# Kernel tuning notes

Hardware: AMD Instinct MI355X
Metric: run time of the kernel (lower is better)

## Reference

```python
import jax, jax.numpy as jnp
import numpy as np

C = 128        # attention channels (inner_channel)
OUT_C = 256    # bottleneck output channels (in_channel)
NEG = -10000000.0


def conv_bn_relu(x, W, scale, shift):
    """1x1 conv (no bias) + eval-mode BatchNorm folded to scale/shift + ReLU.
    x: [B, Cin, H, W], W: [Cout, Cin]."""
    y = jnp.einsum('oc,bchw->bohw', W, x)
    y = y * scale[None, :, None, None] + shift[None, :, None, None]
    return jax.nn.relu(y)


def setup_inputs() -> dict:
    key = jax.random.key(0)
    ks = jax.random.split(key, 20)
    B, H, W_, K = 4, 128, 128, 1024
    inp = {
        'query_feats': jax.random.normal(ks[0], (B, C, H, W_), jnp.float32),
        'key_feats':   jax.random.normal(ks[1], (B, C, K, 1), jnp.float32),
        'value_feats': jax.random.normal(ks[2], (B, C, K, 1), jnp.float32),
        'key_mask':    jax.random.randint(ks[3], (B, 1, K, 1), 0, 2).astype(bool),
    }
    s = 1.0 / np.sqrt(C)

    def mk(i, cin, cout):
        return (jax.random.normal(ks[i], (cout, cin), jnp.float32) * s,
                jnp.ones((cout,), jnp.float32),
                jnp.zeros((cout,), jnp.float32))

    inp['Wq1'], inp['sq1'], inp['bq1'] = mk(4, C, C)
    inp['Wq2'], inp['sq2'], inp['bq2'] = mk(5, C, C)
    inp['Wk1'], inp['sk1'], inp['bk1'] = mk(6, C, C)
    inp['Wk2'], inp['sk2'], inp['bk2'] = mk(7, C, C)
    inp['Wv'],  inp['sv'],  inp['bv']  = mk(8, C, C)
    inp['Wo'],  inp['so'],  inp['bo']  = mk(9, C, C)
    inp['Wb'],  inp['sb'],  inp['bb']  = mk(10, 2 * C, OUT_C)
    return inp


def reference(query_feats, key_feats, value_feats, key_mask,
              Wq1, sq1, bq1, Wq2, sq2, bq2,
              Wk1, sk1, bk1, Wk2, sk2, bk2,
              Wv, sv, bv, Wo, so, bo, Wb, sb, bb):
    B, _, H, W_ = query_feats.shape
    # projections (2 conv-bn-relu for q/k, 1 for v)
    q = conv_bn_relu(conv_bn_relu(query_feats, Wq1, sq1, bq1), Wq2, sq2, bq2)
    k = conv_bn_relu(conv_bn_relu(key_feats, Wk1, sk1, bk1), Wk2, sk2, bk2)
    v = conv_bn_relu(value_feats, Wv, sv, bv)

    q = q.reshape(B, C, -1).transpose(0, 2, 1)   # [B, HW, C]
    k = k.reshape(B, C, -1)                      # [B, C, K]
    v = v.reshape(B, C, -1).transpose(0, 2, 1)   # [B, K, C]

    sim = jnp.einsum('bqc,bck->bqk', q, k) * (C ** -0.5)   # [B, HW, K]
    m = key_mask.reshape(B, 1, -1).astype(sim.dtype)        # [B, 1, K]
    sim = sim * m + NEG * (1.0 - m)
    attn = jax.nn.softmax(sim, axis=-1)

    ctx = jnp.einsum('bqk,bkc->bqc', attn, v)               # [B, HW, C]
    ctx = ctx.transpose(0, 2, 1).reshape(B, C, H, W_)
    ctx = conv_bn_relu(ctx, Wo, so, bo)                     # out_project

    out = conv_bn_relu(jnp.concatenate([ctx, query_feats], axis=1), Wb, sb, bb)
    return out
```

## Files before the change

### kernel.cpp

```cpp
#include <hip/hip_runtime.h>
#include <hip/hip_bf16.h>

#define B_    4
#define C_    128
#define HW_   16384
#define K_    1024
#define NEG_  (-10000000.0f)
#define SCALE_ 0.08838834764831845f

using bf16 = __hip_bfloat16;
typedef __bf16 b8v __attribute__((ext_vector_type(8)));
typedef __bf16 b4v __attribute__((ext_vector_type(4)));
typedef __bf16 b2v __attribute__((ext_vector_type(2)));
typedef float  f4v __attribute__((ext_vector_type(4)));

__device__ __forceinline__ b8v ldb8(const void* p) { return *(const b8v*)p; }
__device__ __forceinline__ b4v ldb4(const void* p) { return *(const b4v*)p; }
__device__ __forceinline__ void storev(float* p, float v) { *p = v; }
__device__ __forceinline__ void storev(bf16* p, float v)  { *p = __float2bfloat16(v); }

#define XSTRIDE 272

__global__ __launch_bounds__(256) void wprep_kernel(
    const float* __restrict__ Wq1, const float* __restrict__ sq1,
    const float* __restrict__ Wq2, const float* __restrict__ sq2,
    const float* __restrict__ Wo,  const float* __restrict__ so,
    const float* __restrict__ Wb,  const float* __restrict__ sb,
    __bf16* __restrict__ Wq1p, __bf16* __restrict__ Wq2p,
    __bf16* __restrict__ Wop,  __bf16* __restrict__ Wbp)
{
    const int idx = blockIdx.x * 256 + threadIdx.x;
    if (idx < 16384)      { Wq1p[idx] = (__bf16)(Wq1[idx] * sq1[idx >> 7]); }
    else if (idx < 32768) { const int i = idx - 16384; Wq2p[i] = (__bf16)(Wq2[i] * sq2[i >> 7]); }
    else if (idx < 49152) { const int i = idx - 32768; Wop[i]  = (__bf16)(Wo[i]  * so[i >> 7]); }
    else                  { const int i = idx - 49152; Wbp[i]  = (__bf16)(Wb[i]  * sb[i >> 8]); }
}

__global__ __launch_bounds__(256) void tq_kernel(const float* __restrict__ query,
                                                 bf16* __restrict__ qt)
{
    __shared__ float Xs[64 * 129];
    const int p0 = blockIdx.x * 64, b = blockIdx.y, t = threadIdx.x;
    const int pl = t & 63, cg = t >> 6;
#pragma unroll 4
    for (int i = 0; i < 32; ++i) {
        const int c = cg * 32 + i;
        Xs[pl * 129 + c] = query[(size_t)(b * 128 + c) * HW_ + p0 + pl];
    }
    __syncthreads();
#pragma unroll 4
    for (int it = 0; it < 16; ++it) {
        const int p = it * 4 + cg;
        b2v pk;
        pk[0] = (__bf16)Xs[p * 129 + 2 * pl];
        pk[1] = (__bf16)Xs[p * 129 + 2 * pl + 1];
        *(b2v*)(qt + ((size_t)b * HW_ + p0 + p) * 128 + 2 * pl) = pk;
    }
}

__device__ __forceinline__ void layer128_lds(const float* __restrict__ Xs, float* __restrict__ Ysh,
                                             const float* __restrict__ W,
                                             const float* __restrict__ sc, const float* __restrict__ sh)
{
    const int t = threadIdx.x;
    const int o = t & 127;
    const int half = t >> 7;
    float acc[16];
#pragma unroll
    for (int p = 0; p < 16; ++p) acc[p] = 0.f;
    const float* wrow  = W + o * 128;
    const float* xbase = Xs + half * 16;
    for (int c = 0; c < 128; c += 4) {
        const float4 w4 = *(const float4*)(wrow + c);
        const float wj[4] = {w4.x, w4.y, w4.z, w4.w};
#pragma unroll
        for (int j = 0; j < 4; ++j) {
            const float* xr = xbase + (c + j) * 33;
#pragma unroll
            for (int p = 0; p < 16; ++p) acc[p] += wj[j] * xr[p];
        }
    }
    const float s = sc[o], h = sh[o];
    float* yb = Ysh + o * 33 + half * 16;
#pragma unroll
    for (int p = 0; p < 16; ++p) yb[p] = fmaxf(fmaf(s, acc[p], h), 0.f);
}

template <typename OutT>
__device__ __forceinline__ void layer128_store(const float* __restrict__ Xs, OutT* __restrict__ outp,
                                               const float* __restrict__ W,
                                               const float* __restrict__ sc, const float* __restrict__ sh)
{
    const int t = threadIdx.x;
    const int o = t & 127;
    const int half = t >> 7;
    float acc[16];
#pragma unroll
    for (int p = 0; p < 16; ++p) acc[p] = 0.f;
    const float* wrow  = W + o * 128;
    const float* xbase = Xs + half * 16;
    for (int c = 0; c < 128; c += 4) {
        const float4 w4 = *(const float4*)(wrow + c);
        const float wj[4] = {w4.x, w4.y, w4.z, w4.w};
#pragma unroll
        for (int j = 0; j < 4; ++j) {
            const float* xr = xbase + (c + j) * 33;
#pragma unroll
            for (int p = 0; p < 16; ++p) acc[p] += wj[j] * xr[p];
        }
    }
    const float s = sc[o], h = sh[o];
#pragma unroll
    for (int p = 0; p < 16; ++p) {
        float v = fmaxf(fmaf(s, acc[p], h), 0.f);
        storev(&outp[(size_t)(half * 16 + p) * 128 + o], v);
    }
}

__global__ __launch_bounds__(256) void kv_proj_kernel(
    const float* __restrict__ key, const float* __restrict__ val,
    const float* __restrict__ Wk1, const float* __restrict__ sk1, const float* __restrict__ bk1,
    const float* __restrict__ Wk2, const float* __restrict__ sk2, const float* __restrict__ bk2,
    const float* __restrict__ Wv,  const float* __restrict__ sv,  const float* __restrict__ bv,
    bf16* __restrict__ kbuf, bf16* __restrict__ vbuf)
{
    __shared__ __align__(16) float X[128 * 33];
    __shared__ __align__(16) float Y[128 * 33];
    const int p0 = blockIdx.x * 32;
    const int b  = blockIdx.y;
    const int t  = threadIdx.x;

    for (int e = t; e < 4096; e += 256) {
        int c = e >> 5, p = e & 31;
        X[c * 33 + p] = key[(size_t)(b * 128 + c) * K_ + p0 + p];
    }
    __syncthreads();
    layer128_lds(X, Y, Wk1, sk1, bk1);
    __syncthreads();
    layer128_store(Y, kbuf + (size_t)(b * K_ + p0) * 128, Wk2, sk2, bk2);
    __syncthreads();
    for (int e = t; e < 4096; e += 256) {
        int c = e >> 5, p = e & 31;
        X[c * 33 + p] = val[(size_t)(b * 128 + c) * K_ + p0 + p];
    }
    __syncthreads();
    layer128_lds(X, Y, Wv, sv, bv);
    __syncthreads();
    for (int e = t; e < 4096; e += 256) {
        int c = e >> 5, p = e & 31;
        vbuf[(size_t)(b * 128 + c) * K_ + p0 + p] = __float2bfloat16(Y[c * 33 + p]);
    }
}

__global__ __launch_bounds__(256, 2) void qproj_kernel(
    const bf16* __restrict__ qt,
    const __bf16* __restrict__ W1, const float* __restrict__ sh1,
    const __bf16* __restrict__ W2, const float* __restrict__ sh2,
    bf16* __restrict__ qbuf)
{
    __shared__ __align__(16) char Xs[128 * XSTRIDE];
    __shared__ __align__(16) __bf16 Ys[128 * 136];
    const int t = threadIdx.x, w = t >> 6, lane = t & 63;
    const int pl = lane & 15, quad = lane >> 4;
    const int n0 = blockIdx.x * 128, b = blockIdx.y;
    const int ob = 32 * w;

    {
        const char* qg = (const char*)(qt + ((size_t)b * HW_ + n0) * 128) + t * 16;
        char* xl = Xs + (t >> 4) * XSTRIDE + (t & 15) * 16;
#pragma unroll
        for (int i = 0; i < 8; ++i)
            *(float4*)(xl + i * 16 * XSTRIDE) = *(const float4*)(qg + i * 4096);
    }

    b8v W1f[2][4], W2f[2][4];
#pragma unroll
    for (int mt = 0; mt < 2; ++mt)
#pragma unroll
        for (int s = 0; s < 4; ++s) {
            W1f[mt][s] = ldb8(W1 + (ob + mt * 16 + pl) * 128 + s * 32 + quad * 8);
            W2f[mt][s] = ldb8(W2 + (ob + mt * 16 + pl) * 128 + s * 32 + quad * 8);
        }
    __syncthreads();

    f4v acc[2][8];
#pragma unroll
    for (int mt = 0; mt < 2; ++mt)
#pragma unroll
        for (int nt = 0; nt < 8; ++nt) acc[mt][nt] = (f4v){0.f, 0.f, 0.f, 0.f};

#pragma unroll
    for (int s = 0; s < 4; ++s) {
        b8v Bf[8];
#pragma unroll
        for (int nt = 0; nt < 8; ++nt)
            Bf[nt] = ldb8(Xs + (nt * 16 + pl) * XSTRIDE + s * 64 + quad * 16);
#pragma unroll
        for (int mt = 0; mt < 2; ++mt)
#pragma unroll
            for (int nt = 0; nt < 8; ++nt)
                acc[mt][nt] = __builtin_amdgcn_mfma_f32_16x16x32_bf16(W1f[mt][s], Bf[nt], acc[mt][nt], 0, 0, 0);
    }

#pragma unroll
    for (int mt = 0; mt < 2; ++mt) {
        const float4 s4 = *(const float4*)(sh1 + ob + mt * 16 + quad * 4);
        const float shf[4] = {s4.x, s4.y, s4.z, s4.w};
#pragma unroll
        for (int nt = 0; nt < 8; ++nt) {
            b4v y;
#pragma unroll
            for (int r = 0; r < 4; ++r) y[r] = (__bf16)fmaxf(acc[mt][nt][r] + shf[r], 0.f);
            *(b4v*)&Ys[(nt * 16 + pl) * 136 + ob + mt * 16 + quad * 4] = y;
        }
    }
    __syncthreads();

    f4v acc2[2][8];
#pragma unroll
    for (int mt = 0; mt < 2; ++mt)
#pragma unroll
        for (int nt = 0; nt < 8; ++nt) acc2[mt][nt] = (f4v){0.f, 0.f, 0.f, 0.f};

#pragma unroll
    for (int s = 0; s < 4; ++s) {
        b8v Bf[8];
#pragma unroll
        for (int nt = 0; nt < 8; ++nt)
            Bf[nt] = *(const b8v*)&Ys[(nt * 16 + pl) * 136 + s * 32 + quad * 8];
#pragma unroll
        for (int mt = 0; mt < 2; ++mt)
#pragma unroll
            for (int nt = 0; nt < 8; ++nt)
                acc2[mt][nt] = __builtin_amdgcn_mfma_f32_16x16x32_bf16(W2f[mt][s], Bf[nt], acc2[mt][nt], 0, 0, 0);
    }

    bf16* qb = qbuf + ((size_t)b * HW_ + n0) * 128;
#pragma unroll
    for (int mt = 0; mt < 2; ++mt) {
        const float4 s4 = *(const float4*)(sh2 + ob + mt * 16 + quad * 4);
        const float shf[4] = {s4.x, s4.y, s4.z, s4.w};
#pragma unroll
        for (int nt = 0; nt < 8; ++nt) {
            b4v y;
#pragma unroll
            for (int r = 0; r < 4; ++r) y[r] = (__bf16)fmaxf(acc2[mt][nt][r] + shf[r], 0.f);
            *(b4v*)(qb + (size_t)(nt * 16 + pl) * 128 + ob + mt * 16 + quad * 4) = y;
        }
    }
}

#define KSTRIDE 272
#define VSTRIDE 136
__global__ __launch_bounds__(256, 2) void attn_kernel(
    const bf16* __restrict__ qbuf, const bf16* __restrict__ kbuf, const bf16* __restrict__ vbuf,
    const int* __restrict__ mask, bf16* __restrict__ ctxbuf)
{
    __shared__ __align__(16) float bias[K_];
    __shared__ __align__(16) char ktile[64 * KSTRIDE];
    __shared__ __align__(16) char vtile[128 * VSTRIDE];

    const int t    = threadIdx.x;
    const int w    = t >> 6;
    const int lane = t & 63;
    const int m    = lane & 15;
    const int quad = lane >> 4;
    const int q0   = blockIdx.x * 64;
    const int b    = blockIdx.y;

    for (int i = t; i < K_; i += 256)
        bias[i] = (mask[b * K_ + i] != 0) ? 0.f : NEG_;

    b8v qf[4];
    {
        const bf16* qrow = qbuf + ((size_t)b * HW_ + q0 + w * 16 + m) * 128;
#pragma unroll
        for (int s = 0; s < 4; ++s) qf[s] = ldb8(qrow + s * 32 + quad * 8);
    }

    const bf16* kpt = kbuf + (size_t)b * K_ * 128;
    const bf16* vpt = vbuf + (size_t)b * 128 * K_;

    const char* kg = (const char*)kpt + t * 16;
    const char* vg = (const char*)(vpt + (size_t)(t >> 3) * K_) + (t & 7) * 16;
    char* kl = ktile + (t >> 4) * KSTRIDE + (t & 15) * 16;
    char* vl = vtile + (t >> 3) * VSTRIDE + (t & 7) * 16;

    float4 k_r0 = *(const float4*)(kg);
    float4 k_r1 = *(const float4*)(kg + 4096);
    float4 k_r2 = *(const float4*)(kg + 8192);
    float4 k_r3 = *(const float4*)(kg + 12288);
    float4 v_r0 = *(const float4*)(vg);
    float4 v_r1 = *(const float4*)(vg + 65536);
    float4 v_r2 = *(const float4*)(vg + 131072);
    float4 v_r3 = *(const float4*)(vg + 196608);

    f4v acc[8];
#pragma unroll
    for (int i = 0; i < 8; ++i) acc[i] = (f4v){0.f, 0.f, 0.f, 0.f};
    float mrun = -3.0e38f, lrun = 0.f;

    for (int chunk = 0; chunk < 16; ++chunk) {
        const int k0 = chunk * 64;

        *(float4*)(kl)                = k_r0;
        *(float4*)(kl + 16 * KSTRIDE) = k_r1;
        *(float4*)(kl + 32 * KSTRIDE) = k_r2;
        *(float4*)(kl + 48 * KSTRIDE) = k_r3;
        *(float4*)(vl)                = v_r0;
        *(float4*)(vl + 32 * VSTRIDE) = v_r1;
        *(float4*)(vl + 64 * VSTRIDE) = v_r2;
        *(float4*)(vl + 96 * VSTRIDE) = v_r3;
        __syncthreads();

        if (chunk < 15) {
            const char* kgn = kg + (chunk + 1) * 16384;
            const char* vgn = vg + (chunk + 1) * 128;
            k_r0 = *(const float4*)(kgn);
            k_r1 = *(const float4*)(kgn + 4096);
            k_r2 = *(const float4*)(kgn + 8192);
            k_r3 = *(const float4*)(kgn + 12288);
            v_r0 = *(const float4*)(vgn);
            v_r1 = *(const float4*)(vgn + 65536);
            v_r2 = *(const float4*)(vgn + 131072);
            v_r3 = *(const float4*)(vgn + 196608);
        }

        f4v sv[4];
#pragma unroll
        for (int kt = 0; kt < 4; ++kt) {
            f4v a = (f4v){0.f, 0.f, 0.f, 0.f};
            const char* krow = ktile + (kt * 16 + m) * KSTRIDE + quad * 16;
#pragma unroll
            for (int s = 0; s < 4; ++s)
                a = __builtin_amdgcn_mfma_f32_16x16x32_bf16(ldb8(krow + s * 64), qf[s], a, 0, 0, 0);
            const float4 b4 = *(const float4*)&bias[k0 + kt * 16 + quad * 4];
            const float bb4[4] = {b4.x, b4.y, b4.z, b4.w};
#pragma unroll
            for (int r = 0; r < 4; ++r) sv[kt][r] = a[r] * SCALE_ + bb4[r];
        }

        float mloc = sv[0][0];
#pragma unroll
        for (int kt = 0; kt < 4; ++kt)
#pragma unroll
            for (int r = 0; r < 4; ++r) mloc = fmaxf(mloc, sv[kt][r]);
        mloc = fmaxf(mloc, __shfl_xor(mloc, 16, 64));
        mloc = fmaxf(mloc, __shfl_xor(mloc, 32, 64));
        const float mn = fmaxf(mrun, mloc);
        const float alpha = __expf(mrun - mn);
        mrun = mn;

        b4v pk[4];
        float rs = 0.f;
#pragma unroll
        for (int kt = 0; kt < 4; ++kt)
#pragma unroll
            for (int r = 0; r < 4; ++r) {
                const float p = __expf(sv[kt][r] - mn);
                rs += p;
                pk[kt][r] = (__bf16)p;
            }
        rs += __shfl_xor(rs, 16, 64);
        rs += __shfl_xor(rs, 32, 64);
        lrun = lrun * alpha + rs;

        float alr[4];
#pragma unroll
        for (int r = 0; r < 4; ++r) alr[r] = __shfl(alpha, quad * 4 + r, 64);
#pragma unroll
        for (int ct = 0; ct < 8; ++ct)
#pragma unroll
            for (int r = 0; r < 4; ++r) acc[ct][r] *= alr[r];

        const b8v A0 = __builtin_shufflevector(pk[0], pk[1], 0, 1, 2, 3, 4, 5, 6, 7);
        const b8v A1 = __builtin_shufflevector(pk[2], pk[3], 0, 1, 2, 3, 4, 5, 6, 7);
#pragma unroll
        for (int ct = 0; ct < 8; ++ct) {
            const char* vrow = vtile + (ct * 16 + m) * VSTRIDE + quad * 8;
            const b8v B0 = __builtin_shufflevector(ldb4(vrow),      ldb4(vrow + 32), 0, 1, 2, 3, 4, 5, 6, 7);
            const b8v B1 = __builtin_shufflevector(ldb4(vrow + 64), ldb4(vrow + 96), 0, 1, 2, 3, 4, 5, 6, 7);
            acc[ct] = __builtin_amdgcn_mfma_f32_16x16x32_bf16(A0, B0, acc[ct], 0, 0, 0);
            acc[ct] = __builtin_amdgcn_mfma_f32_16x16x32_bf16(A1, B1, acc[ct], 0, 0, 0);
        }
        __syncthreads();
    }

    float inv[4];
#pragma unroll
    for (int r = 0; r < 4; ++r) inv[r] = 1.f / __shfl(lrun, quad * 4 + r, 64);
    bf16* crow = ctxbuf + ((size_t)b * HW_ + q0 + w * 16) * 128;
#pragma unroll
    for (int ct = 0; ct < 8; ++ct)
#pragma unroll
        for (int r = 0; r < 4; ++r)
            crow[(size_t)(quad * 4 + r) * 128 + ct * 16 + m] = __float2bfloat16(acc[ct][r] * inv[r]);
}

__global__ __launch_bounds__(256, 2) void final_kernel(
    const bf16* __restrict__ ctx, const bf16* __restrict__ qt,
    const __bf16* __restrict__ Wop, const float* __restrict__ bo,
    const __bf16* __restrict__ Wbp, const float* __restrict__ bb,
    float* __restrict__ out)
{
    __shared__ __align__(16) char Xs[128 * XSTRIDE];
    __shared__ __align__(16) __bf16 Ys[128 * 136];
    const int t = threadIdx.x, w = t >> 6, lane = t & 63;
    const int pl = lane & 15, quad = lane >> 4;
    const int n0 = blockIdx.x * 128, b = blockIdx.y;
    const int ob = 32 * w;

    char* xl = Xs + (t >> 4) * XSTRIDE + (t & 15) * 16;

    {
        const char* cg = (const char*)(ctx + ((size_t)b * HW_ + n0) * 128) + t * 16;
#pragma unroll
        for (int i = 0; i < 8; ++i)
            *(float4*)(xl + i * 16 * XSTRIDE) = *(const float4*)(cg + i * 4096);
    }

    b8v Wof[2][4];
#pragma unroll
    for (int mt = 0; mt < 2; ++mt)
#pragma unroll
        for (int s = 0; s < 4; ++s)
            Wof[mt][s] = ldb8(Wop + (ob + mt * 16 + pl) * 128 + s * 32 + quad * 8);
    __syncthreads();

    const char* qg = (const char*)(qt + ((size_t)b * HW_ + n0) * 128) + t * 16;
    float4 q_s0 = *(const float4*)(qg);
    float4 q_s1 = *(const float4*)(qg + 4096);
    float4 q_s2 = *(const float4*)(qg + 8192);
    float4 q_s3 = *(const float4*)(qg + 12288);
    float4 q_s4 = *(const float4*)(qg + 16384);
    float4 q_s5 = *(const float4*)(qg + 20480);
    float4 q_s6 = *(const float4*)(qg + 24576);
    float4 q_s7 = *(const float4*)(qg + 28672);

    f4v acc1[2][8];
#pragma unroll
    for (int mt = 0; mt < 2; ++mt)
#pragma unroll
        for (int nt = 0; nt < 8; ++nt) acc1[mt][nt] = (f4v){0.f, 0.f, 0.f, 0.f};

#pragma unroll
    for (int s = 0; s < 4; ++s) {
        b8v Bf[8];
#pragma unroll
        for (int nt = 0; nt < 8; ++nt)
            Bf[nt] = ldb8(Xs + (nt * 16 + pl) * XSTRIDE + s * 64 + quad * 16);
#pragma unroll
        for (int mt = 0; mt < 2; ++mt)
#pragma unroll
            for (int nt = 0; nt < 8; ++nt)
                acc1[mt][nt] = __builtin_amdgcn_mfma_f32_16x16x32_bf16(Wof[mt][s], Bf[nt], acc1[mt][nt], 0, 0, 0);
    }

#pragma unroll
    for (int mt = 0; mt < 2; ++mt) {
        const float4 s4 = *(const float4*)(bo + ob + mt * 16 + quad * 4);
        const float shf[4] = {s4.x, s4.y, s4.z, s4.w};
#pragma unroll
        for (int nt = 0; nt < 8; ++nt) {
            b4v y;
#pragma unroll
            for (int r = 0; r < 4; ++r) y[r] = (__bf16)fmaxf(acc1[mt][nt][r] + shf[r], 0.f);
            *(b4v*)&Ys[(nt * 16 + pl) * 136 + ob + mt * 16 + quad * 4] = y;
        }
    }
    __syncthreads();

    *(float4*)(xl)                 = q_s0;
    *(float4*)(xl + 16 * XSTRIDE)  = q_s1;
    *(float4*)(xl + 32 * XSTRIDE)  = q_s2;
    *(float4*)(xl + 48 * XSTRIDE)  = q_s3;
    *(float4*)(xl + 64 * XSTRIDE)  = q_s4;
    *(float4*)(xl + 80 * XSTRIDE)  = q_s5;
    *(float4*)(xl + 96 * XSTRIDE)  = q_s6;
    *(float4*)(xl + 112 * XSTRIDE) = q_s7;
    __syncthreads();

    f4v acc2[4][8];
#pragma unroll
    for (int mt = 0; mt < 4; ++mt)
#pragma unroll
        for (int nt = 0; nt < 8; ++nt) acc2[mt][nt] = (f4v){0.f, 0.f, 0.f, 0.f};

#pragma unroll
    for (int ks = 0; ks < 8; ++ks) {
        b8v Af[4];
#pragma unroll
        for (int mt = 0; mt < 4; ++mt)
            Af[mt] = ldb8(Wbp + (64 * w + mt * 16 + pl) * 256 + ks * 32 + quad * 8);
        b8v Bf[8];
        if (ks < 4) {
#pragma unroll
            for (int nt = 0; nt < 8; ++nt)
                Bf[nt] = *(const b8v*)&Ys[(nt * 16 + pl) * 136 + ks * 32 + quad * 8];
        } else {
#pragma unroll
            for (int nt = 0; nt < 8; ++nt)
                Bf[nt] = ldb8(Xs + (nt * 16 + pl) * XSTRIDE + (ks - 4) * 64 + quad * 16);
        }
#pragma unroll
        for (int mt = 0; mt < 4; ++mt)
#pragma unroll
            for (int nt = 0; nt < 8; ++nt)
                acc2[mt][nt] = __builtin_amdgcn_mfma_f32_16x16x32_bf16(Af[mt], Bf[nt], acc2[mt][nt], 0, 0, 0);
    }

#pragma unroll
    for (int mt = 0; mt < 4; ++mt) {
        const float4 s4 = *(const float4*)(bb + 64 * w + mt * 16 + quad * 4);
        const float shf[4] = {s4.x, s4.y, s4.z, s4.w};
#pragma unroll
        for (int nt = 0; nt < 8; ++nt)
#pragma unroll
            for (int r = 0; r < 4; ++r)
                out[(size_t)(b * 256 + 64 * w + mt * 16 + quad * 4 + r) * HW_ + n0 + nt * 16 + pl]
                    = fmaxf(acc2[mt][nt][r] + shf[r], 0.f);
    }
}

extern "C" void kernel_launch(void* const* d_in, const int* in_sizes, int n_in,
                              void* d_out, int out_size, void* d_ws, size_t ws_size,
                              hipStream_t stream)
{
    const float* query = (const float*)d_in[0];
    const float* key   = (const float*)d_in[1];
    const float* val   = (const float*)d_in[2];
    const int*   mask  = (const int*)  d_in[3];
    const float* Wq1 = (const float*)d_in[4];  const float* sq1 = (const float*)d_in[5];  const float* bq1 = (const float*)d_in[6];
    const float* Wq2 = (const float*)d_in[7];  const float* sq2 = (const float*)d_in[8];  const float* bq2 = (const float*)d_in[9];
    const float* Wk1 = (const float*)d_in[10]; const float* sk1 = (const float*)d_in[11]; const float* bk1 = (const float*)d_in[12];
    const float* Wk2 = (const float*)d_in[13]; const float* sk2 = (const float*)d_in[14]; const float* bk2 = (const float*)d_in[15];
    const float* Wv  = (const float*)d_in[16]; const float* sv  = (const float*)d_in[17]; const float* bv  = (const float*)d_in[18];
    const float* Wo  = (const float*)d_in[19]; const float* so  = (const float*)d_in[20]; const float* bo  = (const float*)d_in[21];
    const float* Wb  = (const float*)d_in[22]; const float* sb  = (const float*)d_in[23]; const float* bb  = (const float*)d_in[24];

    char* ws = (char*)d_ws;
    bf16*   kbuf = (bf16*)(ws);
    bf16*   vbuf = (bf16*)(ws + (1u << 20));
    bf16*   qbuf = (bf16*)(ws + (2u << 20));
    bf16*   ctxb = (bf16*)(ws + (18u << 20));
    bf16*   qt   = (bf16*)(ws + (34u << 20));
    __bf16* Wq1p = (__bf16*)(ws + (50u << 20));
    __bf16* Wq2p = (__bf16*)(ws + (50u << 20) + (32u << 10));
    __bf16* Wop  = (__bf16*)(ws + (50u << 20) + (64u << 10));
    __bf16* Wbp  = (__bf16*)(ws + (50u << 20) + (96u << 10));
    float* outp = (float*)d_out;

    wprep_kernel<<<448, 256, 0, stream>>>(Wq1, sq1, Wq2, sq2, Wo, so, Wb, sb,
                                          Wq1p, Wq2p, Wop, Wbp);
    tq_kernel<<<dim3(HW_ / 64, B_), 256, 0, stream>>>(query, qt);
    kv_proj_kernel<<<dim3(K_ / 32, B_), 256, 0, stream>>>(
        key, val, Wk1, sk1, bk1, Wk2, sk2, bk2, Wv, sv, bv, kbuf, vbuf);
    qproj_kernel<<<dim3(HW_ / 128, B_), 256, 0, stream>>>(
        qt, Wq1p, bq1, Wq2p, bq2, qbuf);
    attn_kernel<<<dim3(HW_ / 64, B_), 256, 0, stream>>>(
        qbuf, kbuf, vbuf, mask, ctxb);
    final_kernel<<<dim3(HW_ / 128, B_), 256, 0, stream>>>(
        ctxb, qt, Wop, bo, Wbp, bb, outp);
}
```

Baseline: 269.2 us.

## Merge prep kernels into one launch and split final GEMM into two halves

Folds the weight-prep, query-transpose and key/value projection kernels into a single block-indexed prep kernel, removing two launches and letting the independent work run concurrently. In the final kernel, the 256-row bottleneck GEMM is split into two sequential 128-row halves, with each wave holding its Wb fragments for all k-steps in registers. This lowers accumulator register pressure, which may help occupancy, but the Ys/Xs B-fragments are now read twice from LDS. The merged prep kernel uses 33KB of shared memory for every block, including the transpose and weight blocks, which may lower their occupancy.

```diff
diff --git a/kernel.cpp b/kernel.cpp
--- a/kernel.cpp
+++ b/kernel.cpp
@@ -21,43 +21,6 @@
 
 #define XSTRIDE 272
 
-__global__ __launch_bounds__(256) void wprep_kernel(
-    const float* __restrict__ Wq1, const float* __restrict__ sq1,
-    const float* __restrict__ Wq2, const float* __restrict__ sq2,
-    const float* __restrict__ Wo,  const float* __restrict__ so,
-    const float* __restrict__ Wb,  const float* __restrict__ sb,
-    __bf16* __restrict__ Wq1p, __bf16* __restrict__ Wq2p,
-    __bf16* __restrict__ Wop,  __bf16* __restrict__ Wbp)
-{
-    const int idx = blockIdx.x * 256 + threadIdx.x;
-    if (idx < 16384)      { Wq1p[idx] = (__bf16)(Wq1[idx] * sq1[idx >> 7]); }
-    else if (idx < 32768) { const int i = idx - 16384; Wq2p[i] = (__bf16)(Wq2[i] * sq2[i >> 7]); }
-    else if (idx < 49152) { const int i = idx - 32768; Wop[i]  = (__bf16)(Wo[i]  * so[i >> 7]); }
-    else                  { const int i = idx - 49152; Wbp[i]  = (__bf16)(Wb[i]  * sb[i >> 8]); }
-}
-
-__global__ __launch_bounds__(256) void tq_kernel(const float* __restrict__ query,
-                                                 bf16* __restrict__ qt)
-{
-    __shared__ float Xs[64 * 129];
-    const int p0 = blockIdx.x * 64, b = blockIdx.y, t = threadIdx.x;
-    const int pl = t & 63, cg = t >> 6;
-#pragma unroll 4
-    for (int i = 0; i < 32; ++i) {
-        const int c = cg * 32 + i;
-        Xs[pl * 129 + c] = query[(size_t)(b * 128 + c) * HW_ + p0 + pl];
-    }
-    __syncthreads();
-#pragma unroll 4
-    for (int it = 0; it < 16; ++it) {
-        const int p = it * 4 + cg;
-        b2v pk;
-        pk[0] = (__bf16)Xs[p * 129 + 2 * pl];
-        pk[1] = (__bf16)Xs[p * 129 + 2 * pl + 1];
-        *(b2v*)(qt + ((size_t)b * HW_ + p0 + p) * 128 + 2 * pl) = pk;
-    }
-}
-
 __device__ __forceinline__ void layer128_lds(const float* __restrict__ Xs, float* __restrict__ Ysh,
                                              const float* __restrict__ W,
                                              const float* __restrict__ sc, const float* __restrict__ sh)
@@ -117,38 +80,73 @@
     }
 }
 
-__global__ __launch_bounds__(256) void kv_proj_kernel(
-    const float* __restrict__ key, const float* __restrict__ val,
+__global__ __launch_bounds__(256) void prep_kernel(
+    const float* __restrict__ query, const float* __restrict__ key, const float* __restrict__ val,
     const float* __restrict__ Wk1, const float* __restrict__ sk1, const float* __restrict__ bk1,
     const float* __restrict__ Wk2, const float* __restrict__ sk2, const float* __restrict__ bk2,
     const float* __restrict__ Wv,  const float* __restrict__ sv,  const float* __restrict__ bv,
-    bf16* __restrict__ kbuf, bf16* __restrict__ vbuf)
-{
-    __shared__ __align__(16) float X[128 * 33];
-    __shared__ __align__(16) float Y[128 * 33];
-    const int p0 = blockIdx.x * 32;
-    const int b  = blockIdx.y;
-    const int t  = threadIdx.x;
-
-    for (int e = t; e < 4096; e += 256) {
-        int c = e >> 5, p = e & 31;
-        X[c * 33 + p] = key[(size_t)(b * 128 + c) * K_ + p0 + p];
-    }
-    __syncthreads();
-    layer128_lds(X, Y, Wk1, sk1, bk1);
-    __syncthreads();
-    layer128_store(Y, kbuf + (size_t)(b * K_ + p0) * 128, Wk2, sk2, bk2);
-    __syncthreads();
-    for (int e = t; e < 4096; e += 256) {
-        int c = e >> 5, p = e & 31;
-        X[c * 33 + p] = val[(size_t)(b * 128 + c) * K_ + p0 + p];
-    }
-    __syncthreads();
-    layer128_lds(X, Y, Wv, sv, bv);
-    __syncthreads();
-    for (int e = t; e < 4096; e += 256) {
-        int c = e >> 5, p = e & 31;
-        vbuf[(size_t)(b * 128 + c) * K_ + p0 + p] = __float2bfloat16(Y[c * 33 + p]);
+    const float* __restrict__ Wq1, const float* __restrict__ sq1,
+    const float* __restrict__ Wq2, const float* __restrict__ sq2,
+    const float* __restrict__ Wo,  const float* __restrict__ so,
+    const float* __restrict__ Wb,  const float* __restrict__ sb,
+    bf16* __restrict__ qt, bf16* __restrict__ kbuf, bf16* __restrict__ vbuf,
+    __bf16* __restrict__ Wq1p, __bf16* __restrict__ Wq2p,
+    __bf16* __restrict__ Wop,  __bf16* __restrict__ Wbp)
+{
+    __shared__ __align__(16) float S[2 * 128 * 33];
+    const int blk = blockIdx.x;
+    const int t   = threadIdx.x;
+
+    if (blk < 1024) {
+        float* Xs = S;
+        const int p0 = (blk & 255) * 64, b = blk >> 8;
+        const int pl = t & 63, cg = t >> 6;
+#pragma unroll 4
+        for (int i = 0; i < 32; ++i) {
+            const int c = cg * 32 + i;
+            Xs[pl * 129 + c] = query[(size_t)(b * 128 + c) * HW_ + p0 + pl];
+        }
+        __syncthreads();
+#pragma unroll 4
+        for (int it = 0; it < 16; ++it) {
+            const int p = it * 4 + cg;
+            b2v pk;
+            pk[0] = (__bf16)Xs[p * 129 + 2 * pl];
+            pk[1] = (__bf16)Xs[p * 129 + 2 * pl + 1];
+            *(b2v*)(qt + ((size_t)b * HW_ + p0 + p) * 128 + 2 * pl) = pk;
+        }
+    } else if (blk < 1152) {
+        float* X = S;
+        float* Y = S + 128 * 33;
+        const int local = blk - 1024;
+        const int p0 = (local & 31) * 32, b = local >> 5;
+
+        for (int e = t; e < 4096; e += 256) {
+            int c = e >> 5, p = e & 31;
+            X[c * 33 + p] = key[(size_t)(b * 128 + c) * K_ + p0 + p];
+        }
+        __syncthreads();
+        layer128_lds(X, Y, Wk1, sk1, bk1);
+        __syncthreads();
+        layer128_store(Y, kbuf + (size_t)(b * K_ + p0) * 128, Wk2, sk2, bk2);
+        __syncthreads();
+        for (int e = t; e < 4096; e += 256) {
+            int c = e >> 5, p = e & 31;
+            X[c * 33 + p] = val[(size_t)(b * 128 + c) * K_ + p0 + p];
+        }
+        __syncthreads();
+        layer128_lds(X, Y, Wv, sv, bv);
+        __syncthreads();
+        for (int e = t; e < 4096; e += 256) {
+            int c = e >> 5, p = e & 31;
+            vbuf[(size_t)(b * 128 + c) * K_ + p0 + p] = __float2bfloat16(Y[c * 33 + p]);
+        }
+    } else {
+        const int idx = (blk - 1152) * 256 + t;
+        if (idx < 16384)      { Wq1p[idx] = (__bf16)(Wq1[idx] * sq1[idx >> 7]); }
+        else if (idx < 32768) { const int i = idx - 16384; Wq2p[i] = (__bf16)(Wq2[i] * sq2[i >> 7]); }
+        else if (idx < 49152) { const int i = idx - 32768; Wop[i]  = (__bf16)(Wo[i]  * so[i >> 7]); }
+        else                  { const int i = idx - 49152; Wbp[i]  = (__bf16)(Wb[i]  * sb[i >> 8]); }
     }
 }
 
@@ -480,45 +478,53 @@
     *(float4*)(xl + 112 * XSTRIDE) = q_s7;
     __syncthreads();
 
-    f4v acc2[4][8];
-#pragma unroll
-    for (int mt = 0; mt < 4; ++mt)
-#pragma unroll
-        for (int nt = 0; nt < 8; ++nt) acc2[mt][nt] = (f4v){0.f, 0.f, 0.f, 0.f};
-
-#pragma unroll
-    for (int ks = 0; ks < 8; ++ks) {
-        b8v Af[4];
-#pragma unroll
-        for (int mt = 0; mt < 4; ++mt)
-            Af[mt] = ldb8(Wbp + (64 * w + mt * 16 + pl) * 256 + ks * 32 + quad * 8);
-        b8v Bf[8];
-        if (ks < 4) {
+#pragma unroll 1
+    for (int h = 0; h < 2; ++h) {
+        const int mb = 128 * h + 32 * w;
+
+        b8v Wf[2][8];
+#pragma unroll
+        for (int mt = 0; mt < 2; ++mt)
+#pragma unroll
+            for (int ks = 0; ks < 8; ++ks)
+                Wf[mt][ks] = ldb8(Wbp + (size_t)(mb + mt * 16 + pl) * 256 + ks * 32 + quad * 8);
+
+        f4v acc2[2][8];
+#pragma unroll
+        for (int mt = 0; mt < 2; ++mt)
+#pragma unroll
+            for (int nt = 0; nt < 8; ++nt) acc2[mt][nt] = (f4v){0.f, 0.f, 0.f, 0.f};
+
+#pragma unroll
+        for (int ks = 0; ks < 8; ++ks) {
+            b8v Bf[8];
+            if (ks < 4) {
+#pragma unroll
+                for (int nt = 0; nt < 8; ++nt)
+                    Bf[nt] = *(const b8v*)&Ys[(nt * 16 + pl) * 136 + ks * 32 + quad * 8];
+            } else {
+#pragma unroll
+                for (int nt = 0; nt < 8; ++nt)
+                    Bf[nt] = ldb8(Xs + (nt * 16 + pl) * XSTRIDE + (ks - 4) * 64 + quad * 16);
+            }
+#pragma unroll
+            for (int mt = 0; mt < 2; ++mt)
+#pragma unroll
+                for (int nt = 0; nt < 8; ++nt)
+                    acc2[mt][nt] = __builtin_amdgcn_mfma_f32_16x16x32_bf16(Wf[mt][ks], Bf[nt], acc2[mt][nt], 0, 0, 0);
+        }
+
+#pragma unroll
+        for (int mt = 0; mt < 2; ++mt) {
+            const float4 s4 = *(const float4*)(bb + mb + mt * 16 + quad * 4);
+            const float shf[4] = {s4.x, s4.y, s4.z, s4.w};
 #pragma unroll
             for (int nt = 0; nt < 8; ++nt)
-                Bf[nt] = *(const b8v*)&Ys[(nt * 16 + pl) * 136 + ks * 32 + quad * 8];
-        } else {
-#pragma unroll
-            for (int nt = 0; nt < 8; ++nt)
-                Bf[nt] = ldb8(Xs + (nt * 16 + pl) * XSTRIDE + (ks - 4) * 64 + quad * 16);
-        }
-#pragma unroll
-        for (int mt = 0; mt < 4; ++mt)
-#pragma unroll
-            for (int nt = 0; nt < 8; ++nt)
-                acc2[mt][nt] = __builtin_amdgcn_mfma_f32_16x16x32_bf16(Af[mt], Bf[nt], acc2[mt][nt], 0, 0, 0);
-    }
-
-#pragma unroll
-    for (int mt = 0; mt < 4; ++mt) {
-        const float4 s4 = *(const float4*)(bb + 64 * w + mt * 16 + quad * 4);
-        const float shf[4] = {s4.x, s4.y, s4.z, s4.w};
-#pragma unroll
-        for (int nt = 0; nt < 8; ++nt)
-#pragma unroll
-            for (int r = 0; r < 4; ++r)
-                out[(size_t)(b * 256 + 64 * w + mt * 16 + quad * 4 + r) * HW_ + n0 + nt * 16 + pl]
-                    = fmaxf(acc2[mt][nt][r] + shf[r], 0.f);
+#pragma unroll
+                for (int r = 0; r < 4; ++r)
+                    out[(size_t)(b * 256 + mb + mt * 16 + quad * 4 + r) * HW_ + n0 + nt * 16 + pl]
+                        = fmaxf(acc2[mt][nt][r] + shf[r], 0.f);
+        }
     }
 }
 
@@ -550,11 +556,11 @@
     __bf16* Wbp  = (__bf16*)(ws + (50u << 20) + (96u << 10));
     float* outp = (float*)d_out;
 
-    wprep_kernel<<<448, 256, 0, stream>>>(Wq1, sq1, Wq2, sq2, Wo, so, Wb, sb,
-                                          Wq1p, Wq2p, Wop, Wbp);
-    tq_kernel<<<dim3(HW_ / 64, B_), 256, 0, stream>>>(query, qt);
-    kv_proj_kernel<<<dim3(K_ / 32, B_), 256, 0, stream>>>(
-        key, val, Wk1, sk1, bk1, Wk2, sk2, bk2, Wv, sv, bv, kbuf, vbuf);
+    prep_kernel<<<1600, 256, 0, stream>>>(
+        query, key, val,
+        Wk1, sk1, bk1, Wk2, sk2, bk2, Wv, sv, bv,
+        Wq1, sq1, Wq2, sq2, Wo, so, Wb, sb,
+        qt, kbuf, vbuf, Wq1p, Wq2p, Wop, Wbp);
     qproj_kernel<<<dim3(HW_ / 128, B_), 256, 0, stream>>>(
         qt, Wq1p, bq1, Wq2p, bq2, qbuf);
     attn_kernel<<<dim3(HW_ / 64, B_), 256, 0, stream>>>(
```

New measurement: 324.3 us. +20.5%, slower.

## Move K/V projections to bf16 MFMA and merge them into the Q projection launch

Applied to the files above, without the earlier changes.

Replaces the scalar fp32 K/V projection kernel with bf16 MFMA matrix-core work that shares a body with the Q projection. Key and value are transposed to bf16 alongside the query in one transpose kernel, and their weights are prepped with scale folding in the same weight-prep kernel. One launch now handles Q blocks and K/V blocks together, which removes a kernel launch and the slow scalar FMA loop. In exchange, K and V are projected from bf16-rounded inputs, costing some precision, and the KV blocks (two chained projections plus a third) run longer than Q blocks, giving uneven tail work.

```diff
diff --git a/kernel.cpp b/kernel.cpp
--- a/kernel.cpp
+++ b/kernel.cpp
@@ -16,8 +16,6 @@
 
 __device__ __forceinline__ b8v ldb8(const void* p) { return *(const b8v*)p; }
 __device__ __forceinline__ b4v ldb4(const void* p) { return *(const b4v*)p; }
-__device__ __forceinline__ void storev(float* p, float v) { *p = v; }
-__device__ __forceinline__ void storev(bf16* p, float v)  { *p = __float2bfloat16(v); }
 
 #define XSTRIDE 272
 
@@ -26,26 +24,39 @@
     const float* __restrict__ Wq2, const float* __restrict__ sq2,
     const float* __restrict__ Wo,  const float* __restrict__ so,
     const float* __restrict__ Wb,  const float* __restrict__ sb,
+    const float* __restrict__ Wk1, const float* __restrict__ sk1,
+    const float* __restrict__ Wk2, const float* __restrict__ sk2,
+    const float* __restrict__ Wv,  const float* __restrict__ sv,
     __bf16* __restrict__ Wq1p, __bf16* __restrict__ Wq2p,
-    __bf16* __restrict__ Wop,  __bf16* __restrict__ Wbp)
+    __bf16* __restrict__ Wop,  __bf16* __restrict__ Wbp,
+    __bf16* __restrict__ Wk1p, __bf16* __restrict__ Wk2p, __bf16* __restrict__ Wvp)
 {
     const int idx = blockIdx.x * 256 + threadIdx.x;
-    if (idx < 16384)      { Wq1p[idx] = (__bf16)(Wq1[idx] * sq1[idx >> 7]); }
-    else if (idx < 32768) { const int i = idx - 16384; Wq2p[i] = (__bf16)(Wq2[i] * sq2[i >> 7]); }
-    else if (idx < 49152) { const int i = idx - 32768; Wop[i]  = (__bf16)(Wo[i]  * so[i >> 7]); }
-    else                  { const int i = idx - 49152; Wbp[i]  = (__bf16)(Wb[i]  * sb[i >> 8]); }
-}
-
-__global__ __launch_bounds__(256) void tq_kernel(const float* __restrict__ query,
-                                                 bf16* __restrict__ qt)
+    if (idx < 16384)       { Wq1p[idx] = (__bf16)(Wq1[idx] * sq1[idx >> 7]); }
+    else if (idx < 32768)  { const int i = idx - 16384;  Wq2p[i] = (__bf16)(Wq2[i] * sq2[i >> 7]); }
+    else if (idx < 49152)  { const int i = idx - 32768;  Wop[i]  = (__bf16)(Wo[i]  * so[i >> 7]); }
+    else if (idx < 114688) { const int i = idx - 49152;  Wbp[i]  = (__bf16)(Wb[i]  * sb[i >> 8]); }
+    else if (idx < 131072) { const int i = idx - 114688; Wk1p[i] = (__bf16)(Wk1[i] * sk1[i >> 7]); }
+    else if (idx < 147456) { const int i = idx - 131072; Wk2p[i] = (__bf16)(Wk2[i] * sk2[i >> 7]); }
+    else                   { const int i = idx - 147456; Wvp[i]  = (__bf16)(Wv[i]  * sv[i >> 7]); }
+}
+
+__global__ __launch_bounds__(256) void txp_kernel(
+    const float* __restrict__ query, const float* __restrict__ key, const float* __restrict__ val,
+    bf16* __restrict__ qt, bf16* __restrict__ kT, bf16* __restrict__ vT)
 {
     __shared__ float Xs[64 * 129];
-    const int p0 = blockIdx.x * 64, b = blockIdx.y, t = threadIdx.x;
+    const int seg = blockIdx.x, b = blockIdx.y, t = threadIdx.x;
+    const float* src; bf16* dst; int L, p0;
+    if (seg < 256)      { src = query; dst = qt; L = HW_; p0 = seg * 64; }
+    else if (seg < 272) { src = key;   dst = kT; L = K_;  p0 = (seg - 256) * 64; }
+    else                { src = val;   dst = vT; L = K_;  p0 = (seg - 272) * 64; }
+
     const int pl = t & 63, cg = t >> 6;
 #pragma unroll 4
     for (int i = 0; i < 32; ++i) {
         const int c = cg * 32 + i;
-        Xs[pl * 129 + c] = query[(size_t)(b * 128 + c) * HW_ + p0 + pl];
+        Xs[pl * 129 + c] = src[(size_t)(b * 128 + c) * L + p0 + pl];
     }
     __syncthreads();
 #pragma unroll 4
@@ -54,133 +65,145 @@
         b2v pk;
         pk[0] = (__bf16)Xs[p * 129 + 2 * pl];
         pk[1] = (__bf16)Xs[p * 129 + 2 * pl + 1];
-        *(b2v*)(qt + ((size_t)b * HW_ + p0 + p) * 128 + 2 * pl) = pk;
-    }
-}
-
-__device__ __forceinline__ void layer128_lds(const float* __restrict__ Xs, float* __restrict__ Ysh,
-                                             const float* __restrict__ W,
-                                             const float* __restrict__ sc, const float* __restrict__ sh)
-{
-    const int t = threadIdx.x;
-    const int o = t & 127;
-    const int half = t >> 7;
-    float acc[16];
-#pragma unroll
-    for (int p = 0; p < 16; ++p) acc[p] = 0.f;
-    const float* wrow  = W + o * 128;
-    const float* xbase = Xs + half * 16;
-    for (int c = 0; c < 128; c += 4) {
-        const float4 w4 = *(const float4*)(wrow + c);
-        const float wj[4] = {w4.x, w4.y, w4.z, w4.w};
-#pragma unroll
-        for (int j = 0; j < 4; ++j) {
-            const float* xr = xbase + (c + j) * 33;
-#pragma unroll
-            for (int p = 0; p < 16; ++p) acc[p] += wj[j] * xr[p];
-        }
-    }
-    const float s = sc[o], h = sh[o];
-    float* yb = Ysh + o * 33 + half * 16;
-#pragma unroll
-    for (int p = 0; p < 16; ++p) yb[p] = fmaxf(fmaf(s, acc[p], h), 0.f);
-}
-
-template <typename OutT>
-__device__ __forceinline__ void layer128_store(const float* __restrict__ Xs, OutT* __restrict__ outp,
-                                               const float* __restrict__ W,
-                                               const float* __restrict__ sc, const float* __restrict__ sh)
-{
-    const int t = threadIdx.x;
-    const int o = t & 127;
-    const int half = t >> 7;
-    float acc[16];
-#pragma unroll
-    for (int p = 0; p < 16; ++p) acc[p] = 0.f;
-    const float* wrow  = W + o * 128;
-    const float* xbase = Xs + half * 16;
-    for (int c = 0; c < 128; c += 4) {
-        const float4 w4 = *(const float4*)(wrow + c);
-        const float wj[4] = {w4.x, w4.y, w4.z, w4.w};
-#pragma unroll
-        for (int j = 0; j < 4; ++j) {
-            const float* xr = xbase + (c + j) * 33;
-#pragma unroll
-            for (int p = 0; p < 16; ++p) acc[p] += wj[j] * xr[p];
-        }
-    }
-    const float s = sc[o], h = sh[o];
-#pragma unroll
-    for (int p = 0; p < 16; ++p) {
-        float v = fmaxf(fmaf(s, acc[p], h), 0.f);
-        storev(&outp[(size_t)(half * 16 + p) * 128 + o], v);
-    }
-}
-
-__global__ __launch_bounds__(256) void kv_proj_kernel(
-    const float* __restrict__ key, const float* __restrict__ val,
-    const float* __restrict__ Wk1, const float* __restrict__ sk1, const float* __restrict__ bk1,
-    const float* __restrict__ Wk2, const float* __restrict__ sk2, const float* __restrict__ bk2,
-    const float* __restrict__ Wv,  const float* __restrict__ sv,  const float* __restrict__ bv,
-    bf16* __restrict__ kbuf, bf16* __restrict__ vbuf)
-{
-    __shared__ __align__(16) float X[128 * 33];
-    __shared__ __align__(16) float Y[128 * 33];
-    const int p0 = blockIdx.x * 32;
-    const int b  = blockIdx.y;
-    const int t  = threadIdx.x;
-
-    for (int e = t; e < 4096; e += 256) {
-        int c = e >> 5, p = e & 31;
-        X[c * 33 + p] = key[(size_t)(b * 128 + c) * K_ + p0 + p];
-    }
-    __syncthreads();
-    layer128_lds(X, Y, Wk1, sk1, bk1);
-    __syncthreads();
-    layer128_store(Y, kbuf + (size_t)(b * K_ + p0) * 128, Wk2, sk2, bk2);
-    __syncthreads();
-    for (int e = t; e < 4096; e += 256) {
-        int c = e >> 5, p = e & 31;
-        X[c * 33 + p] = val[(size_t)(b * 128 + c) * K_ + p0 + p];
-    }
-    __syncthreads();
-    layer128_lds(X, Y, Wv, sv, bv);
-    __syncthreads();
-    for (int e = t; e < 4096; e += 256) {
-        int c = e >> 5, p = e & 31;
-        vbuf[(size_t)(b * 128 + c) * K_ + p0 + p] = __float2bfloat16(Y[c * 33 + p]);
-    }
-}
-
-__global__ __launch_bounds__(256, 2) void qproj_kernel(
-    const bf16* __restrict__ qt,
+        *(b2v*)(dst + ((size_t)b * L + p0 + p) * 128 + 2 * pl) = pk;
+    }
+}
+
+__device__ __forceinline__ void proj2_body(
+    const bf16* __restrict__ src,
     const __bf16* __restrict__ W1, const float* __restrict__ sh1,
     const __bf16* __restrict__ W2, const float* __restrict__ sh2,
-    bf16* __restrict__ qbuf)
+    bf16* __restrict__ dst, char* Xs, __bf16* Ys)
+{
+    const int t = threadIdx.x, w = t >> 6, lane = t & 63;
+    const int pl = lane & 15, quad = lane >> 4;
+    const int ob = 32 * w;
+
+    {
+        const char* sg = (const char*)src + t * 16;
+        char* xl = Xs + (t >> 4) * XSTRIDE + (t & 15) * 16;
+#pragma unroll
+        for (int i = 0; i < 8; ++i)
+            *(float4*)(xl + i * 16 * XSTRIDE) = *(const float4*)(sg + i * 4096);
+    }
+
+    b8v W1f[2][4], W2f[2][4];
+#pragma unroll
+    for (int mt = 0; mt < 2; ++mt)
+#pragma unroll
+        for (int s = 0; s < 4; ++s) {
+            W1f[mt][s] = ldb8(W1 + (ob + mt * 16 + pl) * 128 + s * 32 + quad * 8);
+            W2f[mt][s] = ldb8(W2 + (ob + mt * 16 + pl) * 128 + s * 32 + quad * 8);
+        }
+    __syncthreads();
+
+    f4v acc[2][8];
+#pragma unroll
+    for (int mt = 0; mt < 2; ++mt)
+#pragma unroll
+        for (int nt = 0; nt < 8; ++nt) acc[mt][nt] = (f4v){0.f, 0.f, 0.f, 0.f};
+
+#pragma unroll
+    for (int s = 0; s < 4; ++s) {
+        b8v Bf[8];
+#pragma unroll
+        for (int nt = 0; nt < 8; ++nt)
+            Bf[nt] = ldb8(Xs + (nt * 16 + pl) * XSTRIDE + s * 64 + quad * 16);
+#pragma unroll
+        for (int mt = 0; mt < 2; ++mt)
+#pragma unroll
+            for (int nt = 0; nt < 8; ++nt)
+                acc[mt][nt] = __builtin_amdgcn_mfma_f32_16x16x32_bf16(W1f[mt][s], Bf[nt], acc[mt][nt], 0, 0, 0);
+    }
+
+#pragma unroll
+    for (int mt = 0; mt < 2; ++mt) {
+        const float4 s4 = *(const float4*)(sh1 + ob + mt * 16 + quad * 4);
+        const float shf[4] = {s4.x, s4.y, s4.z, s4.w};
+#pragma unroll
+        for (int nt = 0; nt < 8; ++nt) {
+            b4v y;
+#pragma unroll
+            for (int r = 0; r < 4; ++r) y[r] = (__bf16)fmaxf(acc[mt][nt][r] + shf[r], 0.f);
+            *(b4v*)&Ys[(nt * 16 + pl) * 136 + ob + mt * 16 + quad * 4] = y;
+        }
+    }
+    __syncthreads();
+
+    f4v acc2[2][8];
+#pragma unroll
+    for (int mt = 0; mt < 2; ++mt)
+#pragma unroll
+        for (int nt = 0; nt < 8; ++nt) acc2[mt][nt] = (f4v){0.f, 0.f, 0.f, 0.f};
+
+#pragma unroll
+    for (int s = 0; s < 4; ++s) {
+        b8v Bf[8];
+#pragma unroll
+        for (int nt = 0; nt < 8; ++nt)
+            Bf[nt] = *(const b8v*)&Ys[(nt * 16 + pl) * 136 + s * 32 + quad * 8];
+#pragma unroll
+        for (int mt = 0; mt < 2; ++mt)
+#pragma unroll
+            for (int nt = 0; nt < 8; ++nt)
+                acc2[mt][nt] = __builtin_amdgcn_mfma_f32_16x16x32_bf16(W2f[mt][s], Bf[nt], acc2[mt][nt], 0, 0, 0);
+    }
+
+#pragma unroll
+    for (int mt = 0; mt < 2; ++mt) {
+        const float4 s4 = *(const float4*)(sh2 + ob + mt * 16 + quad * 4);
+        const float shf[4] = {s4.x, s4.y, s4.z, s4.w};
+#pragma unroll
+        for (int nt = 0; nt < 8; ++nt) {
+            b4v y;
+#pragma unroll
+            for (int r = 0; r < 4; ++r) y[r] = (__bf16)fmaxf(acc2[mt][nt][r] + shf[r], 0.f);
+            *(b4v*)(dst + (size_t)(nt * 16 + pl) * 128 + ob + mt * 16 + quad * 4) = y;
+        }
+    }
+}
+
+__global__ __launch_bounds__(256, 2) void proj_kernel(
+    const bf16* __restrict__ qt, const bf16* __restrict__ kT, const bf16* __restrict__ vT,
+    const __bf16* __restrict__ Wq1p, const float* __restrict__ bq1,
+    const __bf16* __restrict__ Wq2p, const float* __restrict__ bq2,
+    const __bf16* __restrict__ Wk1p, const float* __restrict__ bk1,
+    const __bf16* __restrict__ Wk2p, const float* __restrict__ bk2,
+    const __bf16* __restrict__ Wvp,  const float* __restrict__ bv,
+    bf16* __restrict__ qbuf, bf16* __restrict__ kbuf, bf16* __restrict__ vbuf)
 {
     __shared__ __align__(16) char Xs[128 * XSTRIDE];
     __shared__ __align__(16) __bf16 Ys[128 * 136];
     const int t = threadIdx.x, w = t >> 6, lane = t & 63;
     const int pl = lane & 15, quad = lane >> 4;
-    const int n0 = blockIdx.x * 128, b = blockIdx.y;
+    const int b = blockIdx.y;
+
+    if (blockIdx.x < 128) {
+        const int n0 = blockIdx.x * 128;
+        proj2_body(qt + ((size_t)b * HW_ + n0) * 128, Wq1p, bq1, Wq2p, bq2,
+                   qbuf + ((size_t)b * HW_ + n0) * 128, Xs, Ys);
+        return;
+    }
+
+    const int n0 = (blockIdx.x - 128) * 128;
+    proj2_body(kT + ((size_t)b * K_ + n0) * 128, Wk1p, bk1, Wk2p, bk2,
+               kbuf + ((size_t)b * K_ + n0) * 128, Xs, Ys);
+    __syncthreads();
+
+    {
+        const char* sg = (const char*)(vT + ((size_t)b * K_ + n0) * 128) + t * 16;
+        char* xl = Xs + (t >> 4) * XSTRIDE + (t & 15) * 16;
+#pragma unroll
+        for (int i = 0; i < 8; ++i)
+            *(float4*)(xl + i * 16 * XSTRIDE) = *(const float4*)(sg + i * 4096);
+    }
     const int ob = 32 * w;
-
-    {
-        const char* qg = (const char*)(qt + ((size_t)b * HW_ + n0) * 128) + t * 16;
-        char* xl = Xs + (t >> 4) * XSTRIDE + (t & 15) * 16;
-#pragma unroll
-        for (int i = 0; i < 8; ++i)
-            *(float4*)(xl + i * 16 * XSTRIDE) = *(const float4*)(qg + i * 4096);
-    }
-
-    b8v W1f[2][4], W2f[2][4];
-#pragma unroll
-    for (int mt = 0; mt < 2; ++mt)
-#pragma unroll
-        for (int s = 0; s < 4; ++s) {
-            W1f[mt][s] = ldb8(W1 + (ob + mt * 16 + pl) * 128 + s * 32 + quad * 8);
-            W2f[mt][s] = ldb8(W2 + (ob + mt * 16 + pl) * 128 + s * 32 + quad * 8);
-        }
+    b8v Wf[2][4];
+#pragma unroll
+    for (int mt = 0; mt < 2; ++mt)
+#pragma unroll
+        for (int s = 0; s < 4; ++s)
+            Wf[mt][s] = ldb8(Wvp + (ob + mt * 16 + pl) * 128 + s * 32 + quad * 8);
     __syncthreads();
 
     f4v acc[2][8];
@@ -199,54 +222,20 @@
         for (int mt = 0; mt < 2; ++mt)
 #pragma unroll
             for (int nt = 0; nt < 8; ++nt)
-                acc[mt][nt] = __builtin_amdgcn_mfma_f32_16x16x32_bf16(W1f[mt][s], Bf[nt], acc[mt][nt], 0, 0, 0);
-    }
-
+                acc[mt][nt] = __builtin_amdgcn_mfma_f32_16x16x32_bf16(Wf[mt][s], Bf[nt], acc[mt][nt], 0, 0, 0);
+    }
+
+    bf16* vb = vbuf + (size_t)b * 128 * K_;
 #pragma unroll
     for (int mt = 0; mt < 2; ++mt) {
-        const float4 s4 = *(const float4*)(sh1 + ob + mt * 16 + quad * 4);
+        const float4 s4 = *(const float4*)(bv + ob + mt * 16 + quad * 4);
         const float shf[4] = {s4.x, s4.y, s4.z, s4.w};
 #pragma unroll
-        for (int nt = 0; nt < 8; ++nt) {
-            b4v y;
-#pragma unroll
-            for (int r = 0; r < 4; ++r) y[r] = (__bf16)fmaxf(acc[mt][nt][r] + shf[r], 0.f);
-            *(b4v*)&Ys[(nt * 16 + pl) * 136 + ob + mt * 16 + quad * 4] = y;
-        }
-    }
-    __syncthreads();
-
-    f4v acc2[2][8];
-#pragma unroll
-    for (int mt = 0; mt < 2; ++mt)
-#pragma unroll
-        for (int nt = 0; nt < 8; ++nt) acc2[mt][nt] = (f4v){0.f, 0.f, 0.f, 0.f};
-
-#pragma unroll
-    for (int s = 0; s < 4; ++s) {
-        b8v Bf[8];
-#pragma unroll
         for (int nt = 0; nt < 8; ++nt)
-            Bf[nt] = *(const b8v*)&Ys[(nt * 16 + pl) * 136 + s * 32 + quad * 8];
-#pragma unroll
-        for (int mt = 0; mt < 2; ++mt)
-#pragma unroll
-            for (int nt = 0; nt < 8; ++nt)
-                acc2[mt][nt] = __builtin_amdgcn_mfma_f32_16x16x32_bf16(W2f[mt][s], Bf[nt], acc2[mt][nt], 0, 0, 0);
-    }
-
-    bf16* qb = qbuf + ((size_t)b * HW_ + n0) * 128;
-#pragma unroll
-    for (int mt = 0; mt < 2; ++mt) {
-        const float4 s4 = *(const float4*)(sh2 + ob + mt * 16 + quad * 4);
-        const float shf[4] = {s4.x, s4.y, s4.z, s4.w};
-#pragma unroll
-        for (int nt = 0; nt < 8; ++nt) {
-            b4v y;
-#pragma unroll
-            for (int r = 0; r < 4; ++r) y[r] = (__bf16)fmaxf(acc2[mt][nt][r] + shf[r], 0.f);
-            *(b4v*)(qb + (size_t)(nt * 16 + pl) * 128 + ob + mt * 16 + quad * 4) = y;
-        }
+#pragma unroll
+            for (int r = 0; r < 4; ++r)
+                vb[(size_t)(ob + mt * 16 + quad * 4 + r) * K_ + n0 + nt * 16 + pl]
+                    = __float2bfloat16(fmaxf(acc[mt][nt][r] + shf[r], 0.f));
     }
 }
 
@@ -491,7 +480,7 @@
         b8v Af[4];
 #pragma unroll
         for (int mt = 0; mt < 4; ++mt)
-            Af[mt] = ldb8(Wbp + (64 * w + mt * 16 + pl) * 256 + ks * 32 + quad * 8);
+            Af[mt] = ldb8(Wbp + (size_t)(64 * w + mt * 16 + pl) * 256 + ks * 32 + quad * 8);
         b8v Bf[8];
         if (ks < 4) {
 #pragma unroll
@@ -544,19 +533,25 @@
     bf16*   qbuf = (bf16*)(ws + (2u << 20));
     bf16*   ctxb = (bf16*)(ws + (18u << 20));
     bf16*   qt   = (bf16*)(ws + (34u << 20));
-    __bf16* Wq1p = (__bf16*)(ws + (50u << 20));
-    __bf16* Wq2p = (__bf16*)(ws + (50u << 20) + (32u << 10));
-    __bf16* Wop  = (__bf16*)(ws + (50u << 20) + (64u << 10));
-    __bf16* Wbp  = (__bf16*)(ws + (50u << 20) + (96u << 10));
+    bf16*   kT   = (bf16*)(ws + (50u << 20));
+    bf16*   vT   = (bf16*)(ws + (51u << 20));
+    char*   wbase = ws + (52u << 20);
+    __bf16* Wq1p = (__bf16*)(wbase);
+    __bf16* Wq2p = (__bf16*)(wbase + (32u << 10));
+    __bf16* Wop  = (__bf16*)(wbase + (64u << 10));
+    __bf16* Wbp  = (__bf16*)(wbase + (96u << 10));
+    __bf16* Wk1p = (__bf16*)(wbase + (224u << 10));
+    __bf16* Wk2p = (__bf16*)(wbase + (256u << 10));
+    __bf16* Wvp  = (__bf16*)(wbase + (288u << 10));
     float* outp = (float*)d_out;
 
-    wprep_kernel<<<448, 256, 0, stream>>>(Wq1, sq1, Wq2, sq2, Wo, so, Wb, sb,
-                                          Wq1p, Wq2p, Wop, Wbp);
-    tq_kernel<<<dim3(HW_ / 64, B_), 256, 0, stream>>>(query, qt);
-    kv_proj_kernel<<<dim3(K_ / 32, B_), 256, 0, stream>>>(
-        key, val, Wk1, sk1, bk1, Wk2, sk2, bk2, Wv, sv, bv, kbuf, vbuf);
-    qproj_kernel<<<dim3(HW_ / 128, B_), 256, 0, stream>>>(
-        qt, Wq1p, bq1, Wq2p, bq2, qbuf);
+    wprep_kernel<<<640, 256, 0, stream>>>(
+        Wq1, sq1, Wq2, sq2, Wo, so, Wb, sb, Wk1, sk1, Wk2, sk2, Wv, sv,
+        Wq1p, Wq2p, Wop, Wbp, Wk1p, Wk2p, Wvp);
+    txp_kernel<<<dim3(288, B_), 256, 0, stream>>>(query, key, val, qt, kT, vT);
+    proj_kernel<<<dim3(136, B_), 256, 0, stream>>>(
+        qt, kT, vT, Wq1p, bq1, Wq2p, bq2, Wk1p, bk1, Wk2p, bk2, Wvp, bv,
+        qbuf, kbuf, vbuf);
     attn_kernel<<<dim3(HW_ / 64, B_), 256, 0, stream>>>(
         qbuf, kbuf, vbuf, mask, ctxb);
     final_kernel<<<dim3(HW_ / 128, B_), 256, 0, stream>>>(
```

Result: faster. 247.1 us (-8.2%).
